# Kernel optimization log

Hardware: AMD Instinct MI355X
Metric: run time of the kernel (lower is better)

Reference implementation:

```python
import jax, jax.numpy as jnp
import numpy as np

FILTER_LENGTH = 1024
HOP_LENGTH = 512
CUTOFF = FILTER_LENGTH // 2 + 1  # 513
PAD_AMOUNT = FILTER_LENGTH // 2  # 512


def _make_forward_basis():
    # DFT matrix rows (real stacked over imag, up to Nyquist), windowed by periodic Hann.
    fb = np.fft.fft(np.eye(FILTER_LENGTH))
    fb = np.vstack([np.real(fb[:CUTOFF, :]), np.imag(fb[:CUTOFF, :])])  # [1026, 1024]
    n = np.arange(FILTER_LENGTH)
    # scipy get_window('hann', N, fftbins=True) == periodic Hann
    win = 0.5 * (1.0 - np.cos(2.0 * np.pi * n / FILTER_LENGTH))
    basis = (fb * win[None, :]).astype(np.float32)
    return basis[:, None, :]  # [out_ch=1026, in_ch=1, k=1024]


def setup_inputs() -> dict:
    key = jax.random.key(0)
    audio = jax.random.normal(key, (15360000,), dtype=jnp.float32)
    forward_basis = jnp.asarray(_make_forward_basis())
    return {"audio": audio, "forward_basis": forward_basis}


def reference(audio, forward_basis):
    # [L] -> [1, 1, L + 2*pad] with reflect padding
    x = jnp.pad(audio, (PAD_AMOUNT, PAD_AMOUNT), mode="reflect")[None, None, :]
    # Strided conv1d == windowed DFT per frame; output [1, 1026, n_frames]
    ft = jax.lax.conv_general_dilated(
        x,
        forward_basis,
        window_strides=(HOP_LENGTH,),
        padding="VALID",
        dimension_numbers=("NCH", "OIH", "NCH"),
    )
    real = ft[:, :CUTOFF, :]
    imag = ft[:, CUTOFF:, :]
    return real * real + imag * imag  # power spectrum [1, 513, n_frames]
```

## Files before the change

kernel.cpp:

```cpp
#include <hip/hip_runtime.h>

#define L_AUDIO 15360000
#define PADLEN  15361024
#define FRAMES  30001
#define NBAS    (1026*1024)

#define BM   256
#define BK   64
#define NKT  16
#define NGEMM 472
#define NWG   504

typedef __attribute__((ext_vector_type(8))) short short8;
typedef __attribute__((ext_vector_type(4))) float f32x4;

__device__ __forceinline__ unsigned short f2bf(float f) {
    unsigned int u = __float_as_uint(f);
    u += 0x7fffu + ((u >> 16) & 1u);
    return (unsigned short)(u >> 16);
}

__global__ __launch_bounds__(256) void prep_pad_k(const float* __restrict__ a,
                                                  unsigned short* __restrict__ pad) {
    long i = (long)blockIdx.x * blockDim.x + threadIdx.x;
    long p0 = i * 4;
    if (p0 >= 512 && p0 + 4 <= 512 + L_AUDIO) {
        const float4 v = *reinterpret_cast<const float4*>(a + (p0 - 512));
        ushort4 o;
        o.x = f2bf(v.x); o.y = f2bf(v.y); o.z = f2bf(v.z); o.w = f2bf(v.w);
        *reinterpret_cast<ushort4*>(pad + p0) = o;
    } else {
        for (int j = 0; j < 4; ++j) {
            long p = p0 + j;
            long src = p - 512;
            if (p < 512) src = 512 - p;
            else if (src >= L_AUDIO) src = 2L*L_AUDIO - 2 - src;
            pad[p] = f2bf(a[src]);
        }
    }
}

__global__ __launch_bounds__(256) void prep_bas_k(const float* __restrict__ b,
                                                  unsigned short* __restrict__ o) {
    long i = (long)blockIdx.x * blockDim.x + threadIdx.x;
    const float4 v = *reinterpret_cast<const float4*>(b + i * 4);
    ushort4 u;
    u.x = f2bf(v.x); u.y = f2bf(v.y); u.z = f2bf(v.z); u.w = f2bf(v.w);
    *reinterpret_cast<ushort4*>(o + i * 4) = u;
}

__global__ __launch_bounds__(512, 2) void stft_gemm(const unsigned short* __restrict__ pad,
                                                    const unsigned short* __restrict__ bas,
                                                    const float* __restrict__ bas32,
                                                    float* __restrict__ out) {
    __shared__ unsigned short lsA[2][BM * BK];
    __shared__ unsigned short lsB[2][BM * BK];

    const int tid = threadIdx.x;

    const int bid = blockIdx.x;
    const int wg  = (bid & 7) * 63 + (bid >> 3);

    if (wg >= NGEMM) {
        const int k    = wg - NGEMM;
        const int base = k * 938;
        const int lim  = (base + 938 < FRAMES) ? base + 938 : FRAMES;
        const float* br = bas32 + (long)512  * 1024;
        const float* bi = bas32 + (long)1025 * 1024;
        float* o512 = out + (long)512 * FRAMES;
        #pragma unroll
        for (int rep = 0; rep < 2; ++rep) {
            const int f = base + rep * 512 + tid;
            if (f < lim) {
                const unsigned short* ap = pad + (long)f * 512;
                float re = 0.f, im = 0.f;
                for (int n = 0; n < 1024; n += 8) {
                    short8 a8 = *reinterpret_cast<const short8*>(ap + n);
                    #pragma unroll
                    for (int u = 0; u < 8; ++u) {
                        float av = __uint_as_float(((unsigned)(unsigned short)a8[u]) << 16);
                        re = fmaf(av, br[n + u], re);
                        im = fmaf(av, bi[n + u], im);
                    }
                }
                o512[f] = re * re + im * im;
            }
        }
        return;
    }

    const int w    = tid >> 6;
    const int lane = tid & 63;
    const int l15  = lane & 15;
    const int lk   = lane >> 4;
    const int wm   = w >> 2;
    const int wn   = w & 3;

    const int  fb = wg >> 2;
    const int  cb = wg & 3;
    const long t0 = (long)fb * BM;
    const int  c0 = cb * 128;

    const int sc = (tid & 7) ^ ((tid >> 3) & 7);
    const unsigned short* aS[4];
    #pragma unroll
    for (int j = 0; j < 4; ++j) {
        long tf = t0 + j * 64 + (tid >> 3);
        if (tf > FRAMES - 1) tf = FRAMES - 1;
        aS[j] = pad + tf * 512 + sc * 8;
    }
    const int ch0 = c0 + ((tid >> 8) << 4) + ((tid >> 3) & 15);
    const long brow0 = ch0 + (((tid >> 7) & 1) ? 513 : 0);
    const unsigned short* bS0 = bas + brow0 * 1024 + sc * 8;

    f32x4 acc[8][4];
    #pragma unroll
    for (int a = 0; a < 8; ++a)
        #pragma unroll
        for (int b = 0; b < 4; ++b)
            acc[a][b] = (f32x4){0.f, 0.f, 0.f, 0.f};

    const int wmBase = wm * 128;
    const int wnBase = wn * 64;

#define GLD(dst, src) __builtin_amdgcn_global_load_lds( \
        (const __attribute__((address_space(1))) unsigned int*)(src), \
        (__attribute__((address_space(3))) unsigned int*)(dst), 16, 0, 0)

#define LDSREAD(basePtr, r, S) \
    (*reinterpret_cast<const short8*>(reinterpret_cast<const char*>(basePtr) \
        + (r) * 128 + ((((S) * 4 + lk) ^ ((r) & 7)) << 4)))

    #pragma unroll
    for (int j = 0; j < 4; ++j) {
        GLD(&lsA[0][j * 4096 + tid * 8], aS[j]);
        GLD(&lsB[0][j * 4096 + tid * 8], bS0 + j * 32768);
    }

    for (int t = 0; t < NKT; ++t) {
        const int p = t & 1;
        const unsigned short* curA = lsA[p];
        const unsigned short* curB = lsB[p];

        __syncthreads();

        if (t + 1 < NKT) {
            const int ko = (t + 1) * BK;
            unsigned short* nA = lsA[p ^ 1];
            unsigned short* nB = lsB[p ^ 1];
            #pragma unroll
            for (int j = 0; j < 4; ++j) {
                GLD(nA + j * 4096 + tid * 8, aS[j] + ko);
                GLD(nB + j * 4096 + tid * 8, bS0 + j * 32768 + ko);
            }
        }

        #pragma unroll
        for (int S = 0; S < 2; ++S) {
            short8 bf[4];
            #pragma unroll
            for (int b = 0; b < 4; ++b)
                bf[b] = LDSREAD(curB, wnBase + b * 16 + l15, S);
            #pragma unroll
            for (int mq = 0; mq < 8; ++mq) {
                short8 af = LDSREAD(curA, wmBase + mq * 16 + l15, S);
                #pragma unroll
                for (int b = 0; b < 4; ++b)
                    acc[mq][b] = __builtin_amdgcn_mfma_f32_16x16x32_bf16(
                        af, bf[b], acc[mq][b], 0, 0, 0);
            }
        }
    }

    const int tb = (int)t0 + wmBase;
    #pragma unroll
    for (int a = 0; a < 8; ++a) {
        #pragma unroll
        for (int q = 0; q < 2; ++q) {
            const int ch = c0 + wn * 32 + q * 16 + l15;
            const long ob = (long)ch * FRAMES;
            const int tv = tb + a * 16 + lk * 4;
            const f32x4 re = acc[a][q * 2];
            const f32x4 im = acc[a][q * 2 + 1];
            if (tv + 3 < FRAMES) {
                #pragma unroll
                for (int r = 0; r < 4; ++r)
                    out[ob + tv + r] = re[r] * re[r] + im[r] * im[r];
            } else {
                #pragma unroll
                for (int r = 0; r < 4; ++r)
                    if (tv + r < FRAMES)
                        out[ob + tv + r] = re[r] * re[r] + im[r] * im[r];
            }
        }
    }
}

extern "C" void kernel_launch(void* const* d_in, const int* in_sizes, int n_in,
                              void* d_out, int out_size, void* d_ws, size_t ws_size,
                              hipStream_t stream) {
    const float* audio = (const float*)d_in[0];
    const float* basis = (const float*)d_in[1];
    float* out = (float*)d_out;

    unsigned short* pad = (unsigned short*)d_ws;
    unsigned short* bas = pad + PADLEN;

    prep_pad_k<<<PADLEN / 4 / 256, 256, 0, stream>>>(audio, pad);
    prep_bas_k<<<NBAS / 4 / 256, 256, 0, stream>>>(basis, bas);

    stft_gemm<<<NWG, 512, 0, stream>>>(pad, bas, basis, out);
}
```

Measured before the change: 127.8 us.

## Interleave prefetch loads with phased LDS reads and MFMA blocks using barriers

The K-loop body is split into four phases. Each phase reads half of the A fragments, plus B fragments where needed, into registers and then issues a 4x4 block of MFMAs. The next tile's global-to-LDS loads are spread across the phases, and an explicit vmcnt wait replaces the single __syncthreads. MFMA blocks are wrapped in s_setprio so waves compete less for the matrix units. The aim is to overlap memory traffic with compute more evenly, at the cost of eight workgroup barriers per iteration and a tighter dependence on hand-tuned wait counts.

```diff
diff --git a/kernel.cpp b/kernel.cpp
--- a/kernel.cpp
+++ b/kernel.cpp
@@ -131,45 +131,72 @@
     (*reinterpret_cast<const short8*>(reinterpret_cast<const char*>(basePtr) \
         + (r) * 128 + ((((S) * 4 + lk) ^ ((r) & 7)) << 4)))
 
+#define PHASE_RA(MQ, S) do { _Pragma("unroll") \
+    for (int j = 0; j < 4; ++j) { \
+        const int r = wmBase + ((MQ) * 4 + j) * 16 + l15; \
+        af[j] = LDSREAD(curA, r, S); } } while (0)
+
+#define PHASE_RB(S) do { _Pragma("unroll") \
+    for (int b = 0; b < 4; ++b) { \
+        const int r = wnBase + b * 16 + l15; \
+        bf[b] = LDSREAD(curB, r, S); } } while (0)
+
+#define PHASE_MFMA(MQ) do { \
+    __builtin_amdgcn_s_setprio(1); \
+    _Pragma("unroll") for (int b_ = 0; b_ < 4; ++b_) \
+      _Pragma("unroll") for (int m_ = 0; m_ < 4; ++m_) \
+        acc[(MQ)*4+m_][b_] = __builtin_amdgcn_mfma_f32_16x16x32_bf16( \
+            af[m_], bf[b_], acc[(MQ)*4+m_][b_], 0, 0, 0); \
+    __builtin_amdgcn_s_setprio(0); } while (0)
+
     #pragma unroll
     for (int j = 0; j < 4; ++j) {
         GLD(&lsA[0][j * 4096 + tid * 8], aS[j]);
         GLD(&lsB[0][j * 4096 + tid * 8], bS0 + j * 32768);
     }
+
+    short8 af[4], bf[4];
 
     for (int t = 0; t < NKT; ++t) {
         const int p = t & 1;
         const unsigned short* curA = lsA[p];
         const unsigned short* curB = lsB[p];
-
-        __syncthreads();
-
-        if (t + 1 < NKT) {
-            const int ko = (t + 1) * BK;
-            unsigned short* nA = lsA[p ^ 1];
-            unsigned short* nB = lsB[p ^ 1];
-            #pragma unroll
-            for (int j = 0; j < 4; ++j) {
-                GLD(nA + j * 4096 + tid * 8, aS[j] + ko);
-                GLD(nB + j * 4096 + tid * 8, bS0 + j * 32768 + ko);
-            }
-        }
-
-        #pragma unroll
-        for (int S = 0; S < 2; ++S) {
-            short8 bf[4];
-            #pragma unroll
-            for (int b = 0; b < 4; ++b)
-                bf[b] = LDSREAD(curB, wnBase + b * 16 + l15, S);
-            #pragma unroll
-            for (int mq = 0; mq < 8; ++mq) {
-                short8 af = LDSREAD(curA, wmBase + mq * 16 + l15, S);
-                #pragma unroll
-                for (int b = 0; b < 4; ++b)
-                    acc[mq][b] = __builtin_amdgcn_mfma_f32_16x16x32_bf16(
-                        af, bf[b], acc[mq][b], 0, 0, 0);
-            }
-        }
+        unsigned short* nxtA = lsA[p ^ 1];
+        unsigned short* nxtB = lsB[p ^ 1];
+        const bool more = (t + 1 < NKT);
+        const int ko = (t + 1) * BK;
+
+        if (more) { GLD(nxtA + 0 * 4096 + tid * 8, aS[0] + ko);
+                    GLD(nxtA + 1 * 4096 + tid * 8, aS[1] + ko); }
+        if (more) asm volatile("s_waitcnt vmcnt(2)" ::: "memory");
+        else      asm volatile("s_waitcnt vmcnt(0)" ::: "memory");
+        __builtin_amdgcn_s_barrier();
+
+        PHASE_RA(0, 0); PHASE_RB(0);
+        if (more) { GLD(nxtA + 2 * 4096 + tid * 8, aS[2] + ko);
+                    GLD(nxtA + 3 * 4096 + tid * 8, aS[3] + ko); }
+        __builtin_amdgcn_s_barrier();
+        PHASE_MFMA(0);
+        __builtin_amdgcn_s_barrier();
+
+        PHASE_RA(1, 0);
+        if (more) { GLD(nxtB + 0 * 4096 + tid * 8, bS0 + 0 * 32768 + ko);
+                    GLD(nxtB + 1 * 4096 + tid * 8, bS0 + 1 * 32768 + ko); }
+        __builtin_amdgcn_s_barrier();
+        PHASE_MFMA(1);
+        __builtin_amdgcn_s_barrier();
+
+        PHASE_RA(0, 1); PHASE_RB(1);
+        if (more) { GLD(nxtB + 2 * 4096 + tid * 8, bS0 + 2 * 32768 + ko);
+                    GLD(nxtB + 3 * 4096 + tid * 8, bS0 + 3 * 32768 + ko); }
+        __builtin_amdgcn_s_barrier();
+        PHASE_MFMA(0);
+        __builtin_amdgcn_s_barrier();
+
+        PHASE_RA(1, 1);
+        __builtin_amdgcn_s_barrier();
+        PHASE_MFMA(1);
+        __builtin_amdgcn_s_barrier();
     }
 
     const int tb = (int)t0 + wmBase;
```

Result: faster. 122.2 us (-4.3%).
